# Optimization experiments

Hardware: AMD Instinct MI355X
Metric: run time of the kernel (lower is better)

The kernel has to match this reference:

```python
import jax, jax.numpy as jnp
import numpy as np

TEMPERATURE = 0.1
NUM_RISK_GROUPS = 4
SIM_WEIGHT = 1.0
CONTRAST_WEIGHT = 0.1
NEG = jnp.float32(-1e9)  # finite stand-in for -inf (grad-safe, exp() == 0 in fp32)


def setup_inputs() -> dict:
    key = jax.random.key(0)
    k1, k2, k3, k4 = jax.random.split(key, 4)
    N, D = 8192, 256
    return {
        "log_risks": jax.random.normal(k1, (N,), dtype=jnp.float32),
        "times": jax.random.uniform(k2, (N,), dtype=jnp.float32),
        "censor": jnp.ones((N,), dtype=jnp.int32),
        "wsi_embeddings": jax.random.normal(k3, (N, D), dtype=jnp.float32),
        "omic_embeddings": jax.random.normal(k4, (N, D), dtype=jnp.float32),
    }


def _cox_loss(log_risks, times, censor):
    lr = jnp.clip(log_risks, -10.0, 10.0)
    order = jnp.argsort(-times)  # descending times
    slr = lr[order]
    sc = censor[order]
    # at-risk sum for index i is sum_{j<=i} exp(slr_j) (arange <= i mask) -> cumsum
    at_risk = jnp.cumsum(jnp.exp(slr))
    li = slr - jnp.log(at_risk + 1e-15)
    mask = (sc == 1)
    cnt = jnp.maximum(jnp.sum(mask), 1)
    return -jnp.sum(jnp.where(mask, li, 0.0)) / cnt


def _similarity_loss(a, b):
    na = jnp.maximum(jnp.linalg.norm(a, axis=1), 1e-8)
    nb = jnp.maximum(jnp.linalg.norm(b, axis=1), 1e-8)
    cos = jnp.clip(jnp.sum(a * b, axis=1) / (na * nb), -1.0, 1.0)
    return jnp.mean(1.0 - cos)


def _contrastive_loss(emb, times):
    # NOTE: assumes censor == 1 for all samples (as in setup_inputs), so the
    # uncensored subset is the whole batch and shapes stay static.
    G = NUM_RISK_GROUPS
    q = jnp.quantile(times, jnp.linspace(0.0, 1.0, G + 1))
    # group = #thresholds q[1..G] that t >= ; max bucket clipped to G-1
    groups = jnp.clip(jnp.sum(times[:, None] >= q[None, 1:], axis=1), 0, G - 1)
    z = emb / jnp.maximum(jnp.linalg.norm(emb, axis=1, keepdims=True), 1e-12)
    sim = (z @ z.T) / TEMPERATURE  # [N, N]
    N = emb.shape[0]
    eye = jnp.eye(N, dtype=bool)
    same = groups[:, None] == groups[None, :]
    pos = same & ~eye
    offdiag = ~eye  # pos | neg == all off-diagonal entries
    lse_pos = jax.nn.logsumexp(jnp.where(pos, sim, NEG), axis=1)
    lse_all = jax.nn.logsumexp(jnp.where(offdiag, sim, NEG), axis=1)
    neg_any = jnp.any(~same & ~eye, axis=1)
    valid = jnp.any(pos, axis=1) & neg_any
    loss = -lse_pos + lse_all
    cnt = jnp.maximum(jnp.sum(valid), 1)
    return jnp.sum(jnp.where(valid, loss, 0.0)) / cnt


def reference(log_risks, times, censor, wsi_embeddings, omic_embeddings):
    cox = _cox_loss(log_risks, times, censor)
    sim = _similarity_loss(wsi_embeddings, omic_embeddings)
    c_wsi = _contrastive_loss(wsi_embeddings, times)
    c_omic = _contrastive_loss(omic_embeddings, times)
    contrast = (c_wsi + c_omic) / 2.0
    return cox + SIM_WEIGHT * sim + CONTRAST_WEIGHT * contrast
```

## Files before the change

kernel.cpp:

```cpp
#include <hip/hip_runtime.h>


#define NN 8192
#define DD 256

typedef __attribute__((ext_vector_type(4))) float f32x4;
typedef __attribute__((ext_vector_type(4))) int i32x4;
typedef __attribute__((ext_vector_type(8))) int i32x8;

__device__ inline void gl_lds16(const void* g, void* l) {
  __builtin_amdgcn_global_load_lds(
      (const __attribute__((address_space(1))) unsigned int*)g,
      (__attribute__((address_space(3))) unsigned int*)l, 16, 0, 0);
}

__global__ void __launch_bounds__(256) k_rows(
    const float* __restrict__ lr, const float* __restrict__ times,
    const int* __restrict__ censor,
    const float* __restrict__ wsi, const float* __restrict__ omic,
    unsigned char* __restrict__ pw, unsigned char* __restrict__ po,
    float* __restrict__ pslots, float* __restrict__ gsum) {
  __shared__ __align__(16) float st[1024];
  __shared__ __align__(16) float se[1024];
  __shared__ float red[4][3];
  const int tid = threadIdx.x;
  const int lane = tid & 63;
  const int wv = tid >> 6;
  const int i = blockIdx.x * 4 + wv;

  if (blockIdx.x < 64) {
    ((f32x4*)gsum)[blockIdx.x * 256 + tid] = (f32x4){0.f, 0.f, 0.f, 0.f};
  }

  const float4 w = ((const float4*)(wsi + (size_t)i * DD))[lane];
  const float4 o = ((const float4*)(omic + (size_t)i * DD))[lane];
  float nw = w.x * w.x + w.y * w.y + w.z * w.z + w.w * w.w;
  float no = o.x * o.x + o.y * o.y + o.z * o.z + o.w * o.w;
  float dd = w.x * o.x + w.y * o.y + w.z * o.z + w.w * o.w;
  for (int m = 1; m < 64; m <<= 1) {
    nw += __shfl_xor(nw, m);
    no += __shfl_xor(no, m);
    dd += __shfl_xor(dd, m);
  }
  const float nws = sqrtf(nw), nos = sqrtf(no);

  const float ti = times[i];
  int rk = 0;
  float ar = 0.f;
  for (int c = 0; c < 8; ++c) {
    __syncthreads();
    for (int p = tid; p < 1024; p += 256) {
      float t = times[c * 1024 + p];
      float l = lr[c * 1024 + p];
      st[p] = t;
      se[p] = __expf(fminf(fmaxf(l, -10.f), 10.f));
    }
    __syncthreads();
#pragma unroll 4
    for (int jt = 0; jt < 16; ++jt) {
      const int p = jt * 64 + lane;
      const float t = st[p];
      const float e = se[p];
      const bool c1 = (t < ti) || ((t == ti) && ((c * 1024 + p) < i));
      rk += c1 ? 1 : 0;
      ar += c1 ? 0.f : e;
    }
  }
  for (int m = 1; m < 64; m <<= 1) {
    rk += __shfl_xor(rk, m);
    ar += __shfl_xor(ar, m);
  }

  if (lane == 0) {
    float c = dd / (fmaxf(nws, 1e-8f) * fmaxf(nos, 1e-8f));
    c = fminf(fmaxf(c, -1.f), 1.f);
    float l = fminf(fmaxf(lr[i], -10.f), 10.f);
    float li = l - logf(ar + 1e-15f);
    bool cen = (censor[i] == 1);
    red[wv][0] = cen ? li : 0.f;
    red[wv][1] = cen ? 1.f : 0.f;
    red[wv][2] = 1.f - c;
  }

  const int r = rk;
  const float iw = 1.f / fmaxf(nws, 1e-12f);
  const float io = 1.f / fmaxf(nos, 1e-12f);
  int zw = __builtin_amdgcn_cvt_pk_fp8_f32(w.x * iw, w.y * iw, 0, false);
  zw = __builtin_amdgcn_cvt_pk_fp8_f32(w.z * iw, w.w * iw, zw, true);
  int zo = __builtin_amdgcn_cvt_pk_fp8_f32(o.x * io, o.y * io, 0, false);
  zo = __builtin_amdgcn_cvt_pk_fp8_f32(o.z * io, o.w * io, zo, true);
  const size_t off = ((size_t)((lane >> 5) * 4 + ((lane >> 3) & 3)) * NN + r) * 32
                     + (lane & 7) * 4;
  *(unsigned int*)(pw + off) = (unsigned int)zw;
  *(unsigned int*)(po + off) = (unsigned int)zo;
  __syncthreads();
  if (tid < 3) {
    pslots[blockIdx.x * 4 + tid] =
        red[0][tid] + red[1][tid] + red[2][tid] + red[3][tid];
  }
}

__global__ void __launch_bounds__(256, 4) k_contrast(
    const unsigned char* __restrict__ pw, const unsigned char* __restrict__ po,
    float* __restrict__ gsum) {
  __shared__ __align__(16) unsigned char sbuf[2][16384];
  const int tid = threadIdx.x;
  const int lane = tid & 63;
  const int wv = tid >> 6;
  const int lo = lane & 15, q = lane >> 4;
  const int cb = blockIdx.x, rb = blockIdx.y, mz = blockIdx.z;
  const unsigned char* __restrict__ pk = (mz == 0) ? pw : po;
  const int rowbase = rb * 128 + wv * 32;
  const int colstart = cb * 512;
  const int g = cb >> 2;

  i32x8 afrag[2][2];
#pragma unroll
  for (int rt = 0; rt < 2; ++rt) {
    const size_t row = rowbase + rt * 16 + lo;
#pragma unroll
    for (int ks = 0; ks < 2; ++ks)
      afrag[rt][ks] = *(const i32x8*)(pk + ((size_t)(ks * 4 + q) * NN + row) * 32);
  }

  const unsigned char* gsrc[4];
#pragma unroll
  for (int p = 0; p < 4; ++p) {
    const int u = (wv * 4 + p) * 64 + lane;
    const int uct = u >> 8, uks = (u >> 7) & 1, uh = (u >> 6) & 1;
    const int ul = u & 63;
    gsrc[p] = pk + ((size_t)(uks * 4 + (ul >> 4)) * NN
                    + colstart + uct * 16 + (ul & 15)) * 32 + uh * 16;
  }
  unsigned char* const ldb = &sbuf[0][(size_t)wv * 4096];

#pragma unroll
  for (int p = 0; p < 4; ++p) gl_lds16(gsrc[p], ldb + p * 1024);
  __syncthreads();

  float s[2][4] = {{0.f}};
  const int dctbase = (wv & 1) * 2;

#pragma unroll 1
  for (int st = 0; st < 8; ++st) {
    if (st < 7) {
      const size_t adv = (size_t)(st + 1) * 2048;
      const size_t bofs = ((st + 1) & 1) ? 16384 : 0;
#pragma unroll
      for (int p = 0; p < 4; ++p) gl_lds16(gsrc[p] + adv, ldb + bofs + p * 1024);
    }
    const unsigned char* buf = &sbuf[st & 1][0];
    const bool diagw = ((rowbase >> 6) == ((colstart + st * 64) >> 6));
#pragma unroll
    for (int ct = 0; ct < 4; ++ct) {
      f32x4 a0 = {0.f, 0.f, 0.f, 0.f}, a1 = {0.f, 0.f, 0.f, 0.f};
#pragma unroll
      for (int ks = 0; ks < 2; ++ks) {
        const int rbase = ((ct * 2 + ks) * 2) * 1024 + lane * 16;
        i32x4 blo = *(const i32x4*)&buf[rbase];
        i32x4 bhi = *(const i32x4*)&buf[rbase + 1024];
        i32x8 b = __builtin_shufflevector(blo, bhi, 0, 1, 2, 3, 4, 5, 6, 7);
        a0 = __builtin_amdgcn_mfma_scale_f32_16x16x128_f8f6f4(
            afrag[0][ks], b, a0, 0, 0, 0, 0x7F, 0, 0x7F);
        a1 = __builtin_amdgcn_mfma_scale_f32_16x16x128_f8f6f4(
            afrag[1][ks], b, a1, 0, 0, 0, 0x7F, 0, 0x7F);
      }
      if (diagw) {
#pragma unroll
        for (int r = 0; r < 4; ++r) {
          float e0 = __builtin_amdgcn_exp2f(fmaf(a0[r], 14.4269504f, -14.4269504f));
          float e1 = __builtin_amdgcn_exp2f(fmaf(a1[r], 14.4269504f, -14.4269504f));
          if (ct == dctbase + 0 && lo == q * 4 + r) e0 = 0.f;
          if (ct == dctbase + 1 && lo == q * 4 + r) e1 = 0.f;
          s[0][r] += e0;
          s[1][r] += e1;
        }
      } else {
#pragma unroll
        for (int r = 0; r < 4; ++r) {
          s[0][r] += __builtin_amdgcn_exp2f(fmaf(a0[r], 14.4269504f, -14.4269504f));
          s[1][r] += __builtin_amdgcn_exp2f(fmaf(a1[r], 14.4269504f, -14.4269504f));
        }
      }
    }
    __syncthreads();
  }

#pragma unroll
  for (int rt = 0; rt < 2; ++rt)
#pragma unroll
    for (int r = 0; r < 4; ++r) {
      float v = s[rt][r];
      v += __shfl_xor(v, 1); v += __shfl_xor(v, 2);
      v += __shfl_xor(v, 4); v += __shfl_xor(v, 8);
      if (lo == 0) {
        const int row = rowbase + rt * 16 + q * 4 + r;
        atomicAdd(&gsum[((size_t)mz * NN + row) * 4 + g], v);
      }
    }
}

__global__ void __launch_bounds__(1024) k_finale(
    const float* __restrict__ pslots, const float* __restrict__ gsum,
    float* __restrict__ out) {
  __shared__ float rsum[16][4];
  const int tid = threadIdx.x;
  const int lane = tid & 63, wv = tid >> 6;
  float cox = 0.f, cnt = 0.f, sim = 0.f, con = 0.f;
  for (int b = tid; b < 2048; b += 1024) {
    const float4 v = ((const float4*)pslots)[b];
    cox += v.x; cnt += v.y; sim += v.z;
  }
  for (int idx = tid; idx < 2 * NN; idx += 1024) {
    const float4 v = ((const float4*)gsum)[idx];
    const int row = idx & (NN - 1);
    const int gg = row >> 11;
    const float sg = (gg == 0) ? v.x : (gg == 1) ? v.y : (gg == 2) ? v.z : v.w;
    con += logf(v.x + v.y + v.z + v.w) - logf(sg);
  }
  for (int m = 1; m < 64; m <<= 1) {
    cox += __shfl_xor(cox, m);
    cnt += __shfl_xor(cnt, m);
    sim += __shfl_xor(sim, m);
    con += __shfl_xor(con, m);
  }
  if (lane == 0) {
    rsum[wv][0] = cox; rsum[wv][1] = cnt; rsum[wv][2] = sim; rsum[wv][3] = con;
  }
  __syncthreads();
  if (tid == 0) {
    float c0 = 0.f, c1 = 0.f, c2 = 0.f, c3 = 0.f;
    for (int k = 0; k < 16; ++k) {
      c0 += rsum[k][0]; c1 += rsum[k][1]; c2 += rsum[k][2]; c3 += rsum[k][3];
    }
    out[0] = -c0 / fmaxf(c1, 1.f) + c2 / (float)NN
             + 0.1f * 0.5f * c3 / (float)NN;
  }
}

extern "C" void kernel_launch(void* const* d_in, const int* in_sizes, int n_in,
                              void* d_out, int out_size, void* d_ws, size_t ws_size,
                              hipStream_t stream) {
  const float* lr = (const float*)d_in[0];
  const float* times = (const float*)d_in[1];
  const int* censor = (const int*)d_in[2];
  const float* wsi = (const float*)d_in[3];
  const float* omic = (const float*)d_in[4];
  float* out = (float*)d_out;

  char* ws = (char*)d_ws;
  float* pslots = (float*)ws;
  float* gsum = (float*)(ws + 32768);
  unsigned char* pw = (unsigned char*)(ws + 294912);
  unsigned char* po = (unsigned char*)(ws + 294912 + 2097152);

  k_rows<<<2048, 256, 0, stream>>>(lr, times, censor, wsi, omic, pw, po, pslots, gsum);
  k_contrast<<<dim3(16, 64, 2), 256, 0, stream>>>(pw, po, gsum);
  k_finale<<<1, 1024, 0, stream>>>(pslots, gsum, out);
}
```

Baseline: 146.0 us.

## Load B fragments directly from global into registers, software-pipeline MFMA and exp epilogue

Removes the LDS double buffer and the per-stage block barriers. Each wave now loads its B fragments straight from global memory into registers, prefetching one column tile ahead. The exp/sum epilogue for the previous tile is also deferred so it can overlap the current tile's MFMAs. The trade-off is that data the four waves used to share through LDS is now loaded redundantly from global/L2 by each wave, and register pressure rises.

```diff
diff --git a/kernel.cpp b/kernel.cpp
--- a/kernel.cpp
+++ b/kernel.cpp
@@ -7,12 +7,6 @@
 typedef __attribute__((ext_vector_type(4))) float f32x4;
 typedef __attribute__((ext_vector_type(4))) int i32x4;
 typedef __attribute__((ext_vector_type(8))) int i32x8;
-
-__device__ inline void gl_lds16(const void* g, void* l) {
-  __builtin_amdgcn_global_load_lds(
-      (const __attribute__((address_space(1))) unsigned int*)g,
-      (__attribute__((address_space(3))) unsigned int*)l, 16, 0, 0);
-}
 
 __global__ void __launch_bounds__(256) k_rows(
     const float* __restrict__ lr, const float* __restrict__ times,
@@ -100,10 +94,31 @@
   }
 }
 
+__device__ inline void epi(const f32x4& a0, const f32x4& a1, int t,
+                           int dt0, int dt1, int lo, int q,
+                           float* __restrict__ s0, float* __restrict__ s1) {
+  if (t == dt0 || t == dt1) {
+#pragma unroll
+    for (int r = 0; r < 4; ++r) {
+      float e0 = __builtin_amdgcn_exp2f(fmaf(a0[r], 14.4269504f, -14.4269504f));
+      float e1 = __builtin_amdgcn_exp2f(fmaf(a1[r], 14.4269504f, -14.4269504f));
+      if (t == dt0 && lo == q * 4 + r) e0 = 0.f;
+      if (t == dt1 && lo == q * 4 + r) e1 = 0.f;
+      s0[r] += e0;
+      s1[r] += e1;
+    }
+  } else {
+#pragma unroll
+    for (int r = 0; r < 4; ++r) {
+      s0[r] += __builtin_amdgcn_exp2f(fmaf(a0[r], 14.4269504f, -14.4269504f));
+      s1[r] += __builtin_amdgcn_exp2f(fmaf(a1[r], 14.4269504f, -14.4269504f));
+    }
+  }
+}
+
 __global__ void __launch_bounds__(256, 4) k_contrast(
     const unsigned char* __restrict__ pw, const unsigned char* __restrict__ po,
     float* __restrict__ gsum) {
-  __shared__ __align__(16) unsigned char sbuf[2][16384];
   const int tid = threadIdx.x;
   const int lane = tid & 63;
   const int wv = tid >> 6;
@@ -123,74 +138,49 @@
       afrag[rt][ks] = *(const i32x8*)(pk + ((size_t)(ks * 4 + q) * NN + row) * 32);
   }
 
-  const unsigned char* gsrc[4];
-#pragma unroll
-  for (int p = 0; p < 4; ++p) {
-    const int u = (wv * 4 + p) * 64 + lane;
-    const int uct = u >> 8, uks = (u >> 7) & 1, uh = (u >> 6) & 1;
-    const int ul = u & 63;
-    gsrc[p] = pk + ((size_t)(uks * 4 + (ul >> 4)) * NN
-                    + colstart + uct * 16 + (ul & 15)) * 32 + uh * 16;
-  }
-  unsigned char* const ldb = &sbuf[0][(size_t)wv * 4096];
-
-#pragma unroll
-  for (int p = 0; p < 4; ++p) gl_lds16(gsrc[p], ldb + p * 1024);
-  __syncthreads();
-
-  float s[2][4] = {{0.f}};
-  const int dctbase = (wv & 1) * 2;
-
-#pragma unroll 1
-  for (int st = 0; st < 8; ++st) {
-    if (st < 7) {
-      const size_t adv = (size_t)(st + 1) * 2048;
-      const size_t bofs = ((st + 1) & 1) ? 16384 : 0;
-#pragma unroll
-      for (int p = 0; p < 4; ++p) gl_lds16(gsrc[p] + adv, ldb + bofs + p * 1024);
-    }
-    const unsigned char* buf = &sbuf[st & 1][0];
-    const bool diagw = ((rowbase >> 6) == ((colstart + st * 64) >> 6));
-#pragma unroll
-    for (int ct = 0; ct < 4; ++ct) {
-      f32x4 a0 = {0.f, 0.f, 0.f, 0.f}, a1 = {0.f, 0.f, 0.f, 0.f};
-#pragma unroll
-      for (int ks = 0; ks < 2; ++ks) {
-        const int rbase = ((ct * 2 + ks) * 2) * 1024 + lane * 16;
-        i32x4 blo = *(const i32x4*)&buf[rbase];
-        i32x4 bhi = *(const i32x4*)&buf[rbase + 1024];
-        i32x8 b = __builtin_shufflevector(blo, bhi, 0, 1, 2, 3, 4, 5, 6, 7);
-        a0 = __builtin_amdgcn_mfma_scale_f32_16x16x128_f8f6f4(
-            afrag[0][ks], b, a0, 0, 0, 0, 0x7F, 0, 0x7F);
-        a1 = __builtin_amdgcn_mfma_scale_f32_16x16x128_f8f6f4(
-            afrag[1][ks], b, a1, 0, 0, 0, 0x7F, 0, 0x7F);
-      }
-      if (diagw) {
-#pragma unroll
-        for (int r = 0; r < 4; ++r) {
-          float e0 = __builtin_amdgcn_exp2f(fmaf(a0[r], 14.4269504f, -14.4269504f));
-          float e1 = __builtin_amdgcn_exp2f(fmaf(a1[r], 14.4269504f, -14.4269504f));
-          if (ct == dctbase + 0 && lo == q * 4 + r) e0 = 0.f;
-          if (ct == dctbase + 1 && lo == q * 4 + r) e1 = 0.f;
-          s[0][r] += e0;
-          s[1][r] += e1;
-        }
-      } else {
-#pragma unroll
-        for (int r = 0; r < 4; ++r) {
-          s[0][r] += __builtin_amdgcn_exp2f(fmaf(a0[r], 14.4269504f, -14.4269504f));
-          s[1][r] += __builtin_amdgcn_exp2f(fmaf(a1[r], 14.4269504f, -14.4269504f));
-        }
-      }
-    }
-    __syncthreads();
-  }
+  const unsigned char* const bbase0 =
+      pk + ((size_t)q * NN + colstart + lo) * 32;
+  const unsigned char* const bbase1 =
+      pk + ((size_t)(4 + q) * NN + colstart + lo) * 32;
+
+  const int dt0 = (rowbase - colstart) >> 4;
+  const int dt1 = dt0 + 1;
+
+  float s0[4] = {0.f, 0.f, 0.f, 0.f};
+  float s1[4] = {0.f, 0.f, 0.f, 0.f};
+  f32x4 acc0[2], acc1[2];
+  i32x8 bcur[2], bnxt[2];
+  bcur[0] = *(const i32x8*)bbase0;
+  bcur[1] = *(const i32x8*)bbase1;
+
+#pragma unroll 2
+  for (int t = 0; t < 32; ++t) {
+    const int cur = t & 1, oth = cur ^ 1;
+    if (t < 31) {
+      bnxt[0] = *(const i32x8*)(bbase0 + (size_t)(t + 1) * 512);
+      bnxt[1] = *(const i32x8*)(bbase1 + (size_t)(t + 1) * 512);
+    }
+    f32x4 z = {0.f, 0.f, 0.f, 0.f};
+    acc0[cur] = z; acc1[cur] = z;
+    acc0[cur] = __builtin_amdgcn_mfma_scale_f32_16x16x128_f8f6f4(
+        afrag[0][0], bcur[0], acc0[cur], 0, 0, 0, 0x7F, 0, 0x7F);
+    acc1[cur] = __builtin_amdgcn_mfma_scale_f32_16x16x128_f8f6f4(
+        afrag[1][0], bcur[0], acc1[cur], 0, 0, 0, 0x7F, 0, 0x7F);
+    acc0[cur] = __builtin_amdgcn_mfma_scale_f32_16x16x128_f8f6f4(
+        afrag[0][1], bcur[1], acc0[cur], 0, 0, 0, 0x7F, 0, 0x7F);
+    acc1[cur] = __builtin_amdgcn_mfma_scale_f32_16x16x128_f8f6f4(
+        afrag[1][1], bcur[1], acc1[cur], 0, 0, 0, 0x7F, 0, 0x7F);
+    if (t > 0) epi(acc0[oth], acc1[oth], t - 1, dt0, dt1, lo, q, s0, s1);
+    bcur[0] = bnxt[0];
+    bcur[1] = bnxt[1];
+  }
+  epi(acc0[1], acc1[1], 31, dt0, dt1, lo, q, s0, s1);
 
 #pragma unroll
   for (int rt = 0; rt < 2; ++rt)
 #pragma unroll
     for (int r = 0; r < 4; ++r) {
-      float v = s[rt][r];
+      float v = rt ? s1[r] : s0[r];
       v += __shfl_xor(v, 1); v += __shfl_xor(v, 2);
       v += __shfl_xor(v, 4); v += __shfl_xor(v, 8);
       if (lo == 0) {
```

New measurement: 154.9 us. 1.06x slower.
